# Optimization experiments

Measured on AMD Instinct MI355X. Metric: run time of the kernel, lower is better.

## Reference

```python
import jax, jax.numpy as jnp
import numpy as np

N, NFEAT, NHID, NCLASS, NHEADS = 8192, 512, 64, 16, 4
ALPHA = 0.2          # leaky_relu slope for attention scores
OUT_SLOPE = 0.01     # flax default slope for per-head output leaky_relu
NEG = -9000000000000000.0


def glorot(key, shape):
    fan_in, fan_out = shape[0], shape[1]
    lim = jnp.sqrt(6.0 / (fan_in + fan_out))
    return jax.random.uniform(key, shape, jnp.float32, -lim, lim)


def setup_inputs() -> dict:
    key = jax.random.key(0)
    ks = jax.random.split(key, 6)
    x = jax.random.normal(ks[0], (N, NFEAT), jnp.float32)
    adj = jax.random.randint(ks[1], (N, N), 0, 2, jnp.int32)
    Wh = glorot(ks[2], (NHEADS * NFEAT, NHID)).reshape(NHEADS, NFEAT, NHID)
    ah = glorot(ks[3], (NHEADS * 2 * NHID, 1)).reshape(NHEADS, 2 * NHID, 1)
    Wo = glorot(ks[4], (NHID * NHEADS, NCLASS))
    ao = glorot(ks[5], (2 * NCLASS, 1))
    return {"x": x, "adj": adj, "Wh": Wh, "ah": ah, "Wo": Wo, "ao": ao}


def _gat_layer(x, adj_mask, W, a, score_slope):
    # h: (N, F)
    h = x @ W
    F = h.shape[1]
    # a_input[i,j] = concat(h_i, h_j); a_input @ a == f1[i] + f2[j]
    f1 = h @ a[:F, 0]   # (N,)
    f2 = h @ a[F:, 0]   # (N,)
    e = jax.nn.leaky_relu(f1[:, None] + f2[None, :], negative_slope=score_slope)
    att = jax.nn.softmax(jnp.where(adj_mask, e, NEG), axis=1)  # (N, N)
    return att @ h  # (N, F)


def reference(x, adj, Wh, ah, Wo, ao):
    adj_mask = adj > 0
    heads = []
    for k in range(NHEADS):  # small fixed structural loop
        hp = _gat_layer(x, adj_mask, Wh[k], ah[k], ALPHA)
        heads.append(jax.nn.leaky_relu(hp, negative_slope=OUT_SLOPE))
    xcat = jnp.concatenate(heads, axis=1)  # (N, NHEADS*NHID)
    # output head: concat=False -> return h_prime directly
    return _gat_layer(xcat, adj_mask, Wo, ao, ALPHA)  # (N, NCLASS)
```

## Files before the change

kernel.cpp:

```cpp
#include <hip/hip_runtime.h>
#include <stdint.h>

#define N      8192
#define FEAT   512
#define HID    64
#define NH     4
#define C1     256
#define PCH    80
#define TC     320
#define NCLS   16
#define C2     32
#define IPB    8

typedef __attribute__((ext_vector_type(8))) short bf16x8;
typedef __attribute__((ext_vector_type(4))) float f32x4;

__device__ __forceinline__ float b2f(uint16_t u){
  uint32_t x = ((uint32_t)u) << 16;
  return __builtin_bit_cast(float, x);
}
__device__ __forceinline__ uint16_t f2b(float f){
  uint32_t x = __builtin_bit_cast(uint32_t, f);
  uint32_t r = (x + 0x7fffu + ((x >> 16) & 1u)) >> 16;
  return (uint16_t)r;
}
__device__ __forceinline__ float lrelu(float v, float a){ return fmaxf(v, a * v); }

__global__ void k0_wht(const float* __restrict__ Wh, float* __restrict__ WhT){
  int idx = blockIdx.x * 256 + threadIdx.x;
  int k = idx >> 15;
  int r = idx & 32767;
  int cc = r >> 9, f = r & 511;
  WhT[idx] = Wh[k * 32768 + f * 64 + cc];
}

__global__ __launch_bounds__(256) void k1_h(const float* __restrict__ x,
    const float* __restrict__ WhT, const float* __restrict__ ah,
    uint16_t* __restrict__ H, float* __restrict__ f1, float* __restrict__ f2)
{
  __shared__ float4 xs[IPB][128];
  int t = threadIdx.x;
  int i0 = blockIdx.x * IPB;
  for (int r = t; r < IPB * 128; r += 256){
    int ii = r >> 7, o = r & 127;
    xs[ii][o] = *((const float4*)(x + (size_t)(i0 + ii) * FEAT) + o);
  }
  __syncthreads();
  int k = t >> 6, cc = t & 63;
  const float4* wrow = (const float4*)(WhT + k * 32768 + cc * 512);
  float acc[IPB] = {};
  for (int f4 = 0; f4 < 128; ++f4){
    float4 wv = wrow[f4];
    #pragma unroll
    for (int ii = 0; ii < IPB; ++ii){
      float4 xv = xs[ii][f4];
      acc[ii] += xv.x * wv.x + xv.y * wv.y + xv.z * wv.z + xv.w * wv.w;
    }
  }
  float a1 = ah[k * 128 + cc], a2 = ah[k * 128 + 64 + cc];
  #pragma unroll
  for (int ii = 0; ii < IPB; ++ii){
    int i = i0 + ii;
    H[(size_t)i * C1 + t] = f2b(acc[ii]);
    float c1v = acc[ii] * a1, c2v = acc[ii] * a2;
    #pragma unroll
    for (int off = 32; off; off >>= 1){
      c1v += __shfl_down(c1v, off);
      c2v += __shfl_down(c2v, off);
    }
    if (cc == 0){ f1[k * N + i] = c1v; f2[k * N + i] = c2v; }
  }
}

__global__ void k2a_htT(const uint16_t* __restrict__ H, uint16_t* __restrict__ HT){
  __shared__ uint16_t tile[64][65];
  int bid = blockIdx.x;
  int k = bid & 3, it = bid >> 2;
  int i0 = it * 64;
  int t = threadIdx.x;
  #pragma unroll
  for (int r = 0; r < 4; ++r){
    int ii = r * 16 + (t >> 4);
    int pp = (t & 15) * 4;
    uint2 v = *(const uint2*)(H + (size_t)(i0 + ii) * C1 + k * 64 + pp);
    const uint16_t* s = (const uint16_t*)&v;
    tile[pp + 0][ii] = s[0]; tile[pp + 1][ii] = s[1];
    tile[pp + 2][ii] = s[2]; tile[pp + 3][ii] = s[3];
  }
  __syncthreads();
  #pragma unroll
  for (int r = 0; r < 4; ++r){
    int pp = r * 16 + (t >> 4);
    int ii = (t & 15) * 4;
    uint2 v;
    uint16_t* s = (uint16_t*)&v;
    s[0] = tile[pp][ii + 0]; s[1] = tile[pp][ii + 1];
    s[2] = tile[pp][ii + 2]; s[3] = tile[pp][ii + 3];
    *(uint2*)(HT + (size_t)k * (PCH * N) + (size_t)pp * N + i0 + ii) = v;
  }
}

__global__ void k2b_fill(uint16_t* __restrict__ HT){
  int fidx = blockIdx.x * 256 + threadIdx.x;
  int k = fidx >> 14;
  int rem = fidx & 16383;
  int p = 64 + (rem >> 10);
  int i0 = (rem & 1023) << 3;
  uint32_t w = (p == 64) ? 0x3F803F80u : 0u;
  uint4 v = {w, w, w, w};
  *((uint4*)(HT + (size_t)k * (PCH * N) + (size_t)p * N + i0)) = v;
}

__global__ __launch_bounds__(256, 2) void k3_attA(const int* __restrict__ adj,
    const uint16_t* __restrict__ HT, const float* __restrict__ f1,
    const float* __restrict__ f2, float* __restrict__ accA)
{
  __shared__ uint16_t Pl[NH][64][48];
  __shared__ uint16_t Hl[TC][48];
  __shared__ float f1s[NH][64];

  const int t = threadIdx.x;
  const int ibl = blockIdx.x >> 2;
  const int js = blockIdx.x & 3;
  const int gi0 = ibl * 64;

  { int k = t >> 6, ii = t & 63; f1s[k][ii] = f1[k * N + gi0 + ii]; }

  const int tj   = t & 31;
  const int half = t >> 5;
  const int lane = t & 63;
  const int wid  = t >> 6;
  const int m    = lane & 15;
  const int q    = lane >> 4;

  f32x4 acc[4][5] = {};
  const int* arow0 = adj + (size_t)(gi0 + half) * N + tj;

  for (int jc = 0; jc < 64; ++jc){
    const int gj = js * 2048 + jc * 32;
    float f2v0 = f2[0 * N + gj + tj];
    float f2v1 = f2[1 * N + gj + tj];
    float f2v2 = f2[2 * N + gj + tj];
    float f2v3 = f2[3 * N + gj + tj];
    int av[8];
    #pragma unroll
    for (int r = 0; r < 8; ++r) av[r] = arow0[(size_t)(8 * r) * N + gj];

    __syncthreads();
    #pragma unroll
    for (int r = 0; r < 5; ++r){
      int idx = t + 256 * r;
      int p = idx >> 2, o4 = idx & 3;
      *(uint4*)&Hl[p][o4 * 8] = *(const uint4*)(HT + (size_t)p * N + gj + o4 * 8);
    }
    #pragma unroll
    for (int r = 0; r < 8; ++r){
      int i = half + 8 * r;
      int a = av[r];
      float s0 = f1s[0][i] + f2v0;
      float s1 = f1s[1][i] + f2v1;
      float s2 = f1s[2][i] + f2v2;
      float s3 = f1s[3][i] + f2v3;
      float w0 = (a > 0) ? __expf(lrelu(s0, 0.2f)) : 0.f;
      float w1 = (a > 0) ? __expf(lrelu(s1, 0.2f)) : 0.f;
      float w2 = (a > 0) ? __expf(lrelu(s2, 0.2f)) : 0.f;
      float w3 = (a > 0) ? __expf(lrelu(s3, 0.2f)) : 0.f;
      Pl[0][i][tj] = f2b(w0);
      Pl[1][i][tj] = f2b(w1);
      Pl[2][i][tj] = f2b(w2);
      Pl[3][i][tj] = f2b(w3);
    }
    __syncthreads();

    bf16x8 af[4];
    #pragma unroll
    for (int it = 0; it < 4; ++it)
      af[it] = *(const bf16x8*)&Pl[wid][it * 16 + m][q * 8];
    #pragma unroll
    for (int ct = 0; ct < 5; ++ct){
      bf16x8 bfr = *(const bf16x8*)&Hl[wid * PCH + ct * 16 + m][q * 8];
      #pragma unroll
      for (int it = 0; it < 4; ++it)
        acc[it][ct] = __builtin_amdgcn_mfma_f32_16x16x32_bf16(af[it], bfr, acc[it][ct], 0, 0, 0);
    }
  }

  #pragma unroll
  for (int it = 0; it < 4; ++it)
    #pragma unroll
    for (int ct = 0; ct < 5; ++ct)
      #pragma unroll
      for (int reg = 0; reg < 4; ++reg){
        int gi = gi0 + it * 16 + q * 4 + reg;
        int c  = wid * PCH + ct * 16 + m;
        accA[((size_t)js * N + gi) * TC + c] = acc[it][ct][reg];
      }
}

__global__ void k4_redA(const float* __restrict__ accA, uint16_t* __restrict__ xcat){
  int i = blockIdx.x;
  int t = threadIdx.x;
  int k = t >> 6, cc = t & 63;
  size_t base = (size_t)i * TC + k * PCH;
  float v = 0.f, Z = 0.f;
  #pragma unroll
  for (int js = 0; js < 4; ++js){
    const float* p = accA + (size_t)js * N * TC + base;
    v += p[cc];
    Z += p[64];
  }
  float r = v / Z;
  xcat[(size_t)i * C1 + t] = f2b(lrelu(r, 0.01f));
}

__global__ __launch_bounds__(256) void k5_h2(const uint16_t* __restrict__ xcat,
    const float* __restrict__ Wo, const float* __restrict__ ao,
    uint16_t* __restrict__ h2T, float* __restrict__ f1o, float* __restrict__ f2o)
{
  __shared__ uint16_t xs[16][256];
  int t = threadIdx.x;
  int i0 = blockIdx.x * 16;
  #pragma unroll
  for (int r = 0; r < 2; ++r){
    int idx = t + 256 * r;
    int ii = idx >> 5, o4 = idx & 31;
    *(uint4*)&xs[ii][o4 * 8] = *(const uint4*)(xcat + (size_t)(i0 + ii) * C1 + o4 * 8);
  }
  __syncthreads();
  int ii = t >> 4, c = t & 15;
  float acc = 0.f;
  for (int f = 0; f < 256; ++f)
    acc += b2f(xs[ii][f]) * Wo[f * 16 + c];
  int i = i0 + ii;
  h2T[(size_t)c * N + i] = f2b(acc);
  float u1 = acc * ao[c];
  float u2 = acc * ao[16 + c];
  #pragma unroll
  for (int off = 8; off; off >>= 1){
    u1 += __shfl_down(u1, off, 16);
    u2 += __shfl_down(u2, off, 16);
  }
  if (c == 0){ f1o[i] = u1; f2o[i] = u2; }
  if (t < 16) h2T[(size_t)16 * N + i0 + t] = 0x3F80;
  if (t < 240){
    int p = 17 + t / 16, io = t % 16;
    h2T[(size_t)p * N + i0 + io] = 0;
  }
}

__global__ __launch_bounds__(256) void k6_attB(const int* __restrict__ adj,
    const uint16_t* __restrict__ h2T, const float* __restrict__ f1o,
    const float* __restrict__ f2o, float* __restrict__ accB)
{
  __shared__ uint16_t Pl[64][48];
  __shared__ uint16_t Hl[32][48];
  __shared__ float f1s[64];

  const int t = threadIdx.x;
  const int ibl = blockIdx.x >> 3;
  const int js = blockIdx.x & 7;
  const int gi0 = ibl * 64;
  if (t < 64) f1s[t] = f1o[gi0 + t];

  const int tj = t & 31;
  const int half = t >> 5;
  const int lane = t & 63;
  const int wid = t >> 6;
  const int m = lane & 15;
  const int q = lane >> 4;

  f32x4 acc0 = {0.f, 0.f, 0.f, 0.f}, acc1 = {0.f, 0.f, 0.f, 0.f};
  const int* arow0 = adj + (size_t)(gi0 + half) * N + tj;

  for (int jc = 0; jc < 32; ++jc){
    const int gj = js * 1024 + jc * 32;
    float f2v = f2o[gj + tj];
    int av[8];
    #pragma unroll
    for (int r = 0; r < 8; ++r) av[r] = arow0[(size_t)(8 * r) * N + gj];

    __syncthreads();
    if (t < 128){
      int p = t >> 2, o4 = t & 3;
      *(uint4*)&Hl[p][o4 * 8] = *(const uint4*)(h2T + (size_t)p * N + gj + o4 * 8);
    }
    #pragma unroll
    for (int r = 0; r < 8; ++r){
      int i = half + 8 * r;
      float s = f1s[i] + f2v;
      float w = (av[r] > 0) ? __expf(lrelu(s, 0.2f)) : 0.f;
      Pl[i][tj] = f2b(w);
    }
    __syncthreads();

    bf16x8 af = *(const bf16x8*)&Pl[wid * 16 + m][q * 8];
    bf16x8 b0 = *(const bf16x8*)&Hl[m][q * 8];
    bf16x8 b1 = *(const bf16x8*)&Hl[16 + m][q * 8];
    acc0 = __builtin_amdgcn_mfma_f32_16x16x32_bf16(af, b0, acc0, 0, 0, 0);
    acc1 = __builtin_amdgcn_mfma_f32_16x16x32_bf16(af, b1, acc1, 0, 0, 0);
  }

  #pragma unroll
  for (int reg = 0; reg < 4; ++reg){
    int gi = gi0 + wid * 16 + q * 4 + reg;
    accB[((size_t)js * N + gi) * C2 + m] = acc0[reg];
    accB[((size_t)js * N + gi) * C2 + 16 + m] = acc1[reg];
  }
}

__global__ void k7_redB(const float* __restrict__ accB, float* __restrict__ out){
  int idx = blockIdx.x * 256 + threadIdx.x;
  int i = idx >> 4, c = idx & 15;
  float v = 0.f, Z = 0.f;
  #pragma unroll
  for (int js = 0; js < 8; ++js){
    const float* p = accB + ((size_t)js * N + i) * C2;
    v += p[c];
    Z += p[16];
  }
  out[idx] = v / Z;
}

extern "C" void kernel_launch(void* const* d_in, const int* in_sizes, int n_in,
                              void* d_out, int out_size, void* d_ws, size_t ws_size,
                              hipStream_t stream)
{
  const float* x   = (const float*)d_in[0];
  const int*   adj = (const int*)d_in[1];
  const float* Wh  = (const float*)d_in[2];
  const float* ah  = (const float*)d_in[3];
  const float* Wo  = (const float*)d_in[4];
  const float* ao  = (const float*)d_in[5];
  float* out = (float*)d_out;

  char* ws = (char*)d_ws;
  float*    WhT  = (float*)   (ws);
  uint16_t* H    = (uint16_t*)(ws + 524288);
  uint16_t* HT   = (uint16_t*)(ws + 4718592);
  float*    f1   = (float*)   (ws + 9961472);
  float*    f2   = (float*)   (ws + 10092544);
  float*    accA = (float*)   (ws + 10223616);
  uint16_t* xcat = (uint16_t*)(ws + 52166656);
  uint16_t* h2T  = (uint16_t*)(ws + 56360960);
  float*    f1o  = (float*)   (ws + 56885248);
  float*    f2o  = (float*)   (ws + 56918016);
  float*    accB = (float*)   (ws + 56950784);

  hipLaunchKernelGGL(k0_wht,   dim3(512),  dim3(256), 0, stream, Wh, WhT);
  hipLaunchKernelGGL(k1_h,     dim3(1024), dim3(256), 0, stream, x, WhT, ah, H, f1, f2);
  hipLaunchKernelGGL(k2a_htT,  dim3(512),  dim3(256), 0, stream, H, HT);
  hipLaunchKernelGGL(k2b_fill, dim3(256),  dim3(256), 0, stream, HT);
  hipLaunchKernelGGL(k3_attA,  dim3(512),  dim3(256), 0, stream, adj, HT, f1, f2, accA);
  hipLaunchKernelGGL(k4_redA,  dim3(8192), dim3(256), 0, stream, accA, xcat);
  hipLaunchKernelGGL(k5_h2,    dim3(512),  dim3(256), 0, stream, xcat, Wo, ao, h2T, f1o, f2o);
  hipLaunchKernelGGL(k6_attB,  dim3(1024), dim3(256), 0, stream, adj, h2T, f1o, f2o, accB);
  hipLaunchKernelGGL(k7_redB,  dim3(512),  dim3(256), 0, stream, accB, out);
}
```

Measured before the change: 631.1 us.

## Bit-pack adjacency, factor exp scores, prefetch tiles in attention kernels

Adds a pre-pass that compresses the int32 adjacency matrix into a transposed bitmask. Both attention kernels then read one bit per edge instead of a full int, which removes most of their adjacency traffic. Attention weights are now built as products of precomputed exp(f1)·exp(f2) and exp(0.2f1)·exp(0.2f2), picking the branch by comparing against 1, so no per-edge exp is needed. The first attention kernel is split across head pairs to double the grid, and next-tile loads are software-prefetched into registers. The price is an extra adjacency conversion pass, possible overflow or precision loss in the exp products, and truncating bf16 rounding.

```diff
diff --git a/kernel.cpp b/kernel.cpp
--- a/kernel.cpp
+++ b/kernel.cpp
@@ -8,7 +8,6 @@
 #define C1     256
 #define PCH    80
 #define TC     320
-#define NCLS   16
 #define C2     32
 #define IPB    8
 
@@ -24,7 +23,29 @@
   uint32_t r = (x + 0x7fffu + ((x >> 16) & 1u)) >> 16;
   return (uint16_t)r;
 }
-__device__ __forceinline__ float lrelu(float v, float a){ return fmaxf(v, a * v); }
+__device__ __forceinline__ uint32_t pack_bf2(float a, float b){
+  uint32_t ua = (__builtin_bit_cast(uint32_t, a) + 0x8000u) >> 16;
+  uint32_t ub = (__builtin_bit_cast(uint32_t, b) + 0x8000u) & 0xFFFF0000u;
+  return ua | ub;
+}
+
+__global__ __launch_bounds__(256) void kA_bits(const int* __restrict__ adj, uint32_t* __restrict__ adjbT){
+  int bid = blockIdx.x;
+  int iband = bid & 127, jwq = bid >> 7;
+  int t = threadIdx.x;
+  int i  = iband * 64 + (t & 63);
+  int jw = jwq * 4 + (t >> 6);
+  const int4* ap = (const int4*)(adj + (size_t)i * N + jw * 32);
+  uint32_t w = 0;
+  #pragma unroll
+  for (int e = 0; e < 8; ++e){
+    int4 v = ap[e];
+    uint32_t nib = (uint32_t)(v.x & 1) | ((uint32_t)(v.y & 1) << 1)
+                 | ((uint32_t)(v.z & 1) << 2) | ((uint32_t)(v.w & 1) << 3);
+    w |= nib << (4 * e);
+  }
+  adjbT[(size_t)jw * N + i] = w;
+}
 
 __global__ void k0_wht(const float* __restrict__ Wh, float* __restrict__ WhT){
   int idx = blockIdx.x * 256 + threadIdx.x;
@@ -72,6 +93,14 @@
   }
 }
 
+__global__ void kE_exp(const float* __restrict__ f1, const float* __restrict__ f2,
+                       float2* __restrict__ e1p, float2* __restrict__ e2p){
+  int idx = blockIdx.x * 256 + threadIdx.x;
+  float v1 = f1[idx], v2 = f2[idx];
+  e1p[idx] = make_float2(__expf(v1), __expf(0.2f * v1));
+  e2p[idx] = make_float2(__expf(v2), __expf(0.2f * v2));
+}
+
 __global__ void k2a_htT(const uint16_t* __restrict__ H, uint16_t* __restrict__ HT){
   __shared__ uint16_t tile[64][65];
   int bid = blockIdx.x;
@@ -111,88 +140,137 @@
   *((uint4*)(HT + (size_t)k * (PCH * N) + (size_t)p * N + i0)) = v;
 }
 
-__global__ __launch_bounds__(256, 2) void k3_attA(const int* __restrict__ adj,
-    const uint16_t* __restrict__ HT, const float* __restrict__ f1,
-    const float* __restrict__ f2, float* __restrict__ accA)
+__global__ __launch_bounds__(256) void k3_attA(const uint32_t* __restrict__ adjbT,
+    const uint16_t* __restrict__ HT, const float* __restrict__ e1p,
+    const float* __restrict__ e2p, float* __restrict__ accA)
 {
-  __shared__ uint16_t Pl[NH][64][48];
-  __shared__ uint16_t Hl[TC][48];
-  __shared__ float f1s[NH][64];
-
-  const int t = threadIdx.x;
-  const int ibl = blockIdx.x >> 2;
-  const int js = blockIdx.x & 3;
+  __shared__ uint16_t Pl[2][64][40];
+  __shared__ uint16_t Hl[160][40];
+
+  const int t   = threadIdx.x;
+  const int bid = blockIdx.x;
+  const int js  = bid & 3;
+  const int hp  = (bid >> 2) & 1;
+  const int ibl = bid >> 3;
   const int gi0 = ibl * 64;
 
-  { int k = t >> 6, ii = t & 63; f1s[k][ii] = f1[k * N + gi0 + ii]; }
-
-  const int tj   = t & 31;
-  const int half = t >> 5;
+  const int jp = t & 15;
+  const int rg = t >> 4;
   const int lane = t & 63;
   const int wid  = t >> 6;
+  const int h_w  = wid >> 1;
+  const int ihalf= wid & 1;
   const int m    = lane & 15;
   const int q    = lane >> 4;
 
-  f32x4 acc[4][5] = {};
-  const int* arow0 = adj + (size_t)(gi0 + half) * N + tj;
-
-  for (int jc = 0; jc < 64; ++jc){
-    const int gj = js * 2048 + jc * 32;
-    float f2v0 = f2[0 * N + gj + tj];
-    float f2v1 = f2[1 * N + gj + tj];
-    float f2v2 = f2[2 * N + gj + tj];
-    float f2v3 = f2[3 * N + gj + tj];
-    int av[8];
-    #pragma unroll
-    for (int r = 0; r < 8; ++r) av[r] = arow0[(size_t)(8 * r) * N + gj];
-
-    __syncthreads();
-    #pragma unroll
-    for (int r = 0; r < 5; ++r){
+  float2 e1v[2][4];
+  #pragma unroll
+  for (int h = 0; h < 2; ++h)
+    #pragma unroll
+    for (int rr = 0; rr < 4; ++rr)
+      e1v[h][rr] = ((const float2*)e1p)[(size_t)(hp * 2 + h) * N + gi0 + rg + 16 * rr];
+
+  f32x4 acc[2][5] = {};
+
+  uint4  vht[3];
+  uint32_t mw[4];
+  float4 e2q[2];
+
+  const int NJ = 64;
+  {
+    const int gj = js * 2048;
+    const int jw = gj >> 5;
+    #pragma unroll
+    for (int r = 0; r < 3; ++r){
       int idx = t + 256 * r;
       int p = idx >> 2, o4 = idx & 3;
-      *(uint4*)&Hl[p][o4 * 8] = *(const uint4*)(HT + (size_t)p * N + gj + o4 * 8);
-    }
-    #pragma unroll
-    for (int r = 0; r < 8; ++r){
-      int i = half + 8 * r;
-      int a = av[r];
-      float s0 = f1s[0][i] + f2v0;
-      float s1 = f1s[1][i] + f2v1;
-      float s2 = f1s[2][i] + f2v2;
-      float s3 = f1s[3][i] + f2v3;
-      float w0 = (a > 0) ? __expf(lrelu(s0, 0.2f)) : 0.f;
-      float w1 = (a > 0) ? __expf(lrelu(s1, 0.2f)) : 0.f;
-      float w2 = (a > 0) ? __expf(lrelu(s2, 0.2f)) : 0.f;
-      float w3 = (a > 0) ? __expf(lrelu(s3, 0.2f)) : 0.f;
-      Pl[0][i][tj] = f2b(w0);
-      Pl[1][i][tj] = f2b(w1);
-      Pl[2][i][tj] = f2b(w2);
-      Pl[3][i][tj] = f2b(w3);
-    }
+      if (r < 2 || t < 128)
+        vht[r] = *(const uint4*)(HT + (size_t)(hp * 160 + p) * N + gj + o4 * 8);
+    }
+    #pragma unroll
+    for (int rr = 0; rr < 4; ++rr)
+      mw[rr] = adjbT[(size_t)jw * N + gi0 + rg + 16 * rr];
+    #pragma unroll
+    for (int h = 0; h < 2; ++h)
+      e2q[h] = *(((const float4*)e2p) + (((size_t)(hp * 2 + h) * N + gj) >> 1) + jp);
+  }
+
+  for (int jc = 0; jc < NJ; ++jc){
+    uint32_t pk[2][4];
+    #pragma unroll
+    for (int h = 0; h < 2; ++h){
+      float4 q4 = e2q[h];
+      #pragma unroll
+      for (int rr = 0; rr < 4; ++rr){
+        float2 e1 = e1v[h][rr];
+        float pa = e1.x * q4.x, psa = e1.y * q4.y;
+        float pb = e1.x * q4.z, psb = e1.y * q4.w;
+        float wa = pa > 1.0f ? pa : psa;
+        float wb = pb > 1.0f ? pb : psb;
+        uint32_t sh = mw[rr] >> (2 * jp);
+        wa = (sh & 1u) ? wa : 0.0f;
+        wb = (sh & 2u) ? wb : 0.0f;
+        pk[h][rr] = pack_bf2(wa, wb);
+      }
+    }
+
     __syncthreads();
-
-    bf16x8 af[4];
-    #pragma unroll
-    for (int it = 0; it < 4; ++it)
-      af[it] = *(const bf16x8*)&Pl[wid][it * 16 + m][q * 8];
+    #pragma unroll
+    for (int r = 0; r < 3; ++r){
+      int idx = t + 256 * r;
+      int p = idx >> 2, o4 = idx & 3;
+      if (r < 2 || t < 128)
+        *(uint4*)&Hl[p][o4 * 8] = vht[r];
+    }
+    {
+      uint32_t* Plw = (uint32_t*)Pl;
+      #pragma unroll
+      for (int h = 0; h < 2; ++h)
+        #pragma unroll
+        for (int rr = 0; rr < 4; ++rr)
+          Plw[(h * 64 + rg + 16 * rr) * 20 + jp] = pk[h][rr];
+    }
+    {
+      int jn = (jc + 1 < NJ) ? jc + 1 : jc;
+      const int gj = js * 2048 + jn * 32;
+      const int jw = gj >> 5;
+      #pragma unroll
+      for (int r = 0; r < 3; ++r){
+        int idx = t + 256 * r;
+        int p = idx >> 2, o4 = idx & 3;
+        if (r < 2 || t < 128)
+          vht[r] = *(const uint4*)(HT + (size_t)(hp * 160 + p) * N + gj + o4 * 8);
+      }
+      #pragma unroll
+      for (int rr = 0; rr < 4; ++rr)
+        mw[rr] = adjbT[(size_t)jw * N + gi0 + rg + 16 * rr];
+      #pragma unroll
+      for (int h = 0; h < 2; ++h)
+        e2q[h] = *(((const float4*)e2p) + (((size_t)(hp * 2 + h) * N + gj) >> 1) + jp);
+    }
+    __syncthreads();
+
+    bf16x8 af[2];
+    #pragma unroll
+    for (int it = 0; it < 2; ++it)
+      af[it] = *(const bf16x8*)&Pl[h_w][ihalf * 32 + it * 16 + m][q * 8];
     #pragma unroll
     for (int ct = 0; ct < 5; ++ct){
-      bf16x8 bfr = *(const bf16x8*)&Hl[wid * PCH + ct * 16 + m][q * 8];
-      #pragma unroll
-      for (int it = 0; it < 4; ++it)
+      bf16x8 bfr = *(const bf16x8*)&Hl[h_w * 80 + ct * 16 + m][q * 8];
+      #pragma unroll
+      for (int it = 0; it < 2; ++it)
         acc[it][ct] = __builtin_amdgcn_mfma_f32_16x16x32_bf16(af[it], bfr, acc[it][ct], 0, 0, 0);
     }
   }
 
   #pragma unroll
-  for (int it = 0; it < 4; ++it)
+  for (int it = 0; it < 2; ++it)
     #pragma unroll
     for (int ct = 0; ct < 5; ++ct)
       #pragma unroll
       for (int reg = 0; reg < 4; ++reg){
-        int gi = gi0 + it * 16 + q * 4 + reg;
-        int c  = wid * PCH + ct * 16 + m;
+        int gi = gi0 + ihalf * 32 + it * 16 + q * 4 + reg;
+        int c  = (hp * 2 + h_w) * PCH + ct * 16 + m;
         accA[((size_t)js * N + gi) * TC + c] = acc[it][ct][reg];
       }
 }
@@ -210,12 +288,12 @@
     Z += p[64];
   }
   float r = v / Z;
-  xcat[(size_t)i * C1 + t] = f2b(lrelu(r, 0.01f));
+  xcat[(size_t)i * C1 + t] = f2b(fmaxf(r, 0.01f * r));
 }
 
 __global__ __launch_bounds__(256) void k5_h2(const uint16_t* __restrict__ xcat,
     const float* __restrict__ Wo, const float* __restrict__ ao,
-    uint16_t* __restrict__ h2T, float* __restrict__ f1o, float* __restrict__ f2o)
+    uint16_t* __restrict__ h2T, float2* __restrict__ e1op, float2* __restrict__ e2op)
 {
   __shared__ uint16_t xs[16][256];
   int t = threadIdx.x;
@@ -240,7 +318,10 @@
     u1 += __shfl_down(u1, off, 16);
     u2 += __shfl_down(u2, off, 16);
   }
-  if (c == 0){ f1o[i] = u1; f2o[i] = u2; }
+  if (c == 0){
+    e1op[i] = make_float2(__expf(u1), __expf(0.2f * u1));
+    e2op[i] = make_float2(__expf(u2), __expf(0.2f * u2));
+  }
   if (t < 16) h2T[(size_t)16 * N + i0 + t] = 0x3F80;
   if (t < 240){
     int p = 17 + t / 16, io = t % 16;
@@ -248,64 +329,112 @@
   }
 }
 
-__global__ __launch_bounds__(256) void k6_attB(const int* __restrict__ adj,
-    const uint16_t* __restrict__ h2T, const float* __restrict__ f1o,
-    const float* __restrict__ f2o, float* __restrict__ accB)
+__global__ __launch_bounds__(256) void k6_attB(const uint32_t* __restrict__ adjbT,
+    const uint16_t* __restrict__ h2T, const float* __restrict__ e1op,
+    const float* __restrict__ e2op, float* __restrict__ accB)
 {
-  __shared__ uint16_t Pl[64][48];
-  __shared__ uint16_t Hl[32][48];
-  __shared__ float f1s[64];
-
-  const int t = threadIdx.x;
-  const int ibl = blockIdx.x >> 3;
-  const int js = blockIdx.x & 7;
+  __shared__ uint16_t Pl[64][40];
+  __shared__ uint16_t Hl[32][40];
+
+  const int t   = threadIdx.x;
+  const int bid = blockIdx.x;
+  const int js  = bid & 7;
+  const int ibl = bid >> 3;
   const int gi0 = ibl * 64;
-  if (t < 64) f1s[t] = f1o[gi0 + t];
-
-  const int tj = t & 31;
-  const int half = t >> 5;
+
+  const int jp = t & 15;
+  const int rg = t >> 4;
   const int lane = t & 63;
-  const int wid = t >> 6;
-  const int m = lane & 15;
-  const int q = lane >> 4;
-
-  f32x4 acc0 = {0.f, 0.f, 0.f, 0.f}, acc1 = {0.f, 0.f, 0.f, 0.f};
-  const int* arow0 = adj + (size_t)(gi0 + half) * N + tj;
-
-  for (int jc = 0; jc < 32; ++jc){
-    const int gj = js * 1024 + jc * 32;
-    float f2v = f2o[gj + tj];
-    int av[8];
-    #pragma unroll
-    for (int r = 0; r < 8; ++r) av[r] = arow0[(size_t)(8 * r) * N + gj];
+  const int wid  = t >> 6;
+  const int ihalf= wid & 1;
+  const int chalf= wid >> 1;
+  const int m    = lane & 15;
+  const int q    = lane >> 4;
+
+  float2 e1v[4];
+  #pragma unroll
+  for (int rr = 0; rr < 4; ++rr)
+    e1v[rr] = ((const float2*)e1op)[gi0 + rg + 16 * rr];
+
+  f32x4 acc[2] = {};
+
+  uint4 vht;
+  uint32_t mw[4];
+  float4 e2q;
+
+  const int NJ = 32;
+  {
+    const int gj = js * 1024;
+    const int jw = gj >> 5;
+    if (t < 128){
+      int p = t >> 2, o4 = t & 3;
+      vht = *(const uint4*)(h2T + (size_t)p * N + gj + o4 * 8);
+    }
+    #pragma unroll
+    for (int rr = 0; rr < 4; ++rr)
+      mw[rr] = adjbT[(size_t)jw * N + gi0 + rg + 16 * rr];
+    e2q = *(((const float4*)e2op) + (gj >> 1) + jp);
+  }
+
+  for (int jc = 0; jc < NJ; ++jc){
+    uint32_t pk[4];
+    {
+      float4 q4 = e2q;
+      #pragma unroll
+      for (int rr = 0; rr < 4; ++rr){
+        float2 e1 = e1v[rr];
+        float pa = e1.x * q4.x, psa = e1.y * q4.y;
+        float pb = e1.x * q4.z, psb = e1.y * q4.w;
+        float wa = pa > 1.0f ? pa : psa;
+        float wb = pb > 1.0f ? pb : psb;
+        uint32_t sh = mw[rr] >> (2 * jp);
+        wa = (sh & 1u) ? wa : 0.0f;
+        wb = (sh & 2u) ? wb : 0.0f;
+        pk[rr] = pack_bf2(wa, wb);
+      }
+    }
 
     __syncthreads();
     if (t < 128){
       int p = t >> 2, o4 = t & 3;
-      *(uint4*)&Hl[p][o4 * 8] = *(const uint4*)(h2T + (size_t)p * N + gj + o4 * 8);
-    }
-    #pragma unroll
-    for (int r = 0; r < 8; ++r){
-      int i = half + 8 * r;
-      float s = f1s[i] + f2v;
-      float w = (av[r] > 0) ? __expf(lrelu(s, 0.2f)) : 0.f;
-      Pl[i][tj] = f2b(w);
+      *(uint4*)&Hl[p][o4 * 8] = vht;
+    }
+    {
+      uint32_t* Plw = (uint32_t*)Pl;
+      #pragma unroll
+      for (int rr = 0; rr < 4; ++rr)
+        Plw[(rg + 16 * rr) * 20 + jp] = pk[rr];
+    }
+    {
+      int jn = (jc + 1 < NJ) ? jc + 1 : jc;
+      const int gj = js * 1024 + jn * 32;
+      const int jw = gj >> 5;
+      if (t < 128){
+        int p = t >> 2, o4 = t & 3;
+        vht = *(const uint4*)(h2T + (size_t)p * N + gj + o4 * 8);
+      }
+      #pragma unroll
+      for (int rr = 0; rr < 4; ++rr)
+        mw[rr] = adjbT[(size_t)jw * N + gi0 + rg + 16 * rr];
+      e2q = *(((const float4*)e2op) + (gj >> 1) + jp);
     }
     __syncthreads();
 
-    bf16x8 af = *(const bf16x8*)&Pl[wid * 16 + m][q * 8];
-    bf16x8 b0 = *(const bf16x8*)&Hl[m][q * 8];
-    bf16x8 b1 = *(const bf16x8*)&Hl[16 + m][q * 8];
-    acc0 = __builtin_amdgcn_mfma_f32_16x16x32_bf16(af, b0, acc0, 0, 0, 0);
-    acc1 = __builtin_amdgcn_mfma_f32_16x16x32_bf16(af, b1, acc1, 0, 0, 0);
-  }
-
-  #pragma unroll
-  for (int reg = 0; reg < 4; ++reg){
-    int gi = gi0 + wid * 16 + q * 4 + reg;
-    accB[((size_t)js * N + gi) * C2 + m] = acc0[reg];
-    accB[((size_t)js * N + gi) * C2 + 16 + m] = acc1[reg];
-  }
+    bf16x8 bfr = *(const bf16x8*)&Hl[chalf * 16 + m][q * 8];
+    #pragma unroll
+    for (int it = 0; it < 2; ++it){
+      bf16x8 af = *(const bf16x8*)&Pl[ihalf * 32 + it * 16 + m][q * 8];
+      acc[it] = __builtin_amdgcn_mfma_f32_16x16x32_bf16(af, bfr, acc[it], 0, 0, 0);
+    }
+  }
+
+  #pragma unroll
+  for (int it = 0; it < 2; ++it)
+    #pragma unroll
+    for (int reg = 0; reg < 4; ++reg){
+      int gi = gi0 + ihalf * 32 + it * 16 + q * 4 + reg;
+      accB[((size_t)js * N + gi) * C2 + chalf * 16 + m] = acc[it][reg];
+    }
 }
 
 __global__ void k7_redB(const float* __restrict__ accB, float* __restrict__ out){
@@ -334,25 +463,30 @@
   float* out = (float*)d_out;
 
   char* ws = (char*)d_ws;
-  float*    WhT  = (float*)   (ws);
-  uint16_t* H    = (uint16_t*)(ws + 524288);
-  uint16_t* HT   = (uint16_t*)(ws + 4718592);
-  float*    f1   = (float*)   (ws + 9961472);
-  float*    f2   = (float*)   (ws + 10092544);
-  float*    accA = (float*)   (ws + 10223616);
-  uint16_t* xcat = (uint16_t*)(ws + 52166656);
-  uint16_t* h2T  = (uint16_t*)(ws + 56360960);
-  float*    f1o  = (float*)   (ws + 56885248);
-  float*    f2o  = (float*)   (ws + 56918016);
-  float*    accB = (float*)   (ws + 56950784);
-
+  float*    WhT   = (float*)   (ws);
+  uint16_t* H     = (uint16_t*)(ws + 524288);
+  uint16_t* HT    = (uint16_t*)(ws + 4718592);
+  float*    f1    = (float*)   (ws + 9961472);
+  float*    f2    = (float*)   (ws + 10092544);
+  float*    accA  = (float*)   (ws + 10223616);
+  uint16_t* xcat  = (uint16_t*)(ws + 52166656);
+  uint16_t* h2T   = (uint16_t*)(ws + 56360960);
+  float2*   e1op  = (float2*)  (ws + 56885248);
+  float2*   e2op  = (float2*)  (ws + 56950784);
+  float*    accB  = (float*)   (ws + 57016320);
+  float2*   e1p   = (float2*)  (ws + 65404928);
+  float2*   e2p   = (float2*)  (ws + 65667072);
+  uint32_t* adjbT = (uint32_t*)(ws + 65929216);
+
+  hipLaunchKernelGGL(kA_bits,  dim3(8192), dim3(256), 0, stream, adj, adjbT);
   hipLaunchKernelGGL(k0_wht,   dim3(512),  dim3(256), 0, stream, Wh, WhT);
   hipLaunchKernelGGL(k1_h,     dim3(1024), dim3(256), 0, stream, x, WhT, ah, H, f1, f2);
+  hipLaunchKernelGGL(kE_exp,   dim3(128),  dim3(256), 0, stream, f1, f2, e1p, e2p);
   hipLaunchKernelGGL(k2a_htT,  dim3(512),  dim3(256), 0, stream, H, HT);
   hipLaunchKernelGGL(k2b_fill, dim3(256),  dim3(256), 0, stream, HT);
-  hipLaunchKernelGGL(k3_attA,  dim3(512),  dim3(256), 0, stream, adj, HT, f1, f2, accA);
+  hipLaunchKernelGGL(k3_attA,  dim3(1024), dim3(256), 0, stream, adjbT, HT, (const float*)e1p, (const float*)e2p, accA);
   hipLaunchKernelGGL(k4_redA,  dim3(8192), dim3(256), 0, stream, accA, xcat);
-  hipLaunchKernelGGL(k5_h2,    dim3(512),  dim3(256), 0, stream, xcat, Wo, ao, h2T, f1o, f2o);
-  hipLaunchKernelGGL(k6_attB,  dim3(1024), dim3(256), 0, stream, adj, h2T, f1o, f2o, accB);
+  hipLaunchKernelGGL(k5_h2,    dim3(512),  dim3(256), 0, stream, xcat, Wo, ao, h2T, e1op, e2op);
+  hipLaunchKernelGGL(k6_attB,  dim3(1024), dim3(256), 0, stream, adjbT, h2T, (const float*)e1op, (const float*)e2op, accB);
   hipLaunchKernelGGL(k7_redB,  dim3(512),  dim3(256), 0, stream, accB, out);
 }
```

New measurement: 740.8 us. 17.4% more time.

## Bit-pack adjacency and factor exp of attention scores into per-node products

Applied to the files above, without the earlier changes.

Adds a pre-pass that packs the int32 adjacency matrix into a transposed bitmask, so both attention kernels read 32x less adjacency data. It rewrites exp(leaky_relu(f1+f2)) as max(e^f1·e^f2, e^{0.2f1}·e^{0.2f2}) using precomputed per-node exponentials, which removes the per-edge exp. The attention kernels now build the MFMA A fragments in registers and load the H fragments straight from global memory, dropping the LDS staging and barriers. The grid is restructured to one head per block. Possible costs are overflow when exponentials are computed separately, and bf16 rounding that now skips the tie-to-even step.

```diff
diff --git a/kernel.cpp b/kernel.cpp
--- a/kernel.cpp
+++ b/kernel.cpp
@@ -8,12 +8,12 @@
 #define C1     256
 #define PCH    80
 #define TC     320
-#define NCLS   16
 #define C2     32
 #define IPB    8
 
 typedef __attribute__((ext_vector_type(8))) short bf16x8;
 typedef __attribute__((ext_vector_type(4))) float f32x4;
+typedef __attribute__((ext_vector_type(4))) uint32_t u32x4;
 
 __device__ __forceinline__ float b2f(uint16_t u){
   uint32_t x = ((uint32_t)u) << 16;
@@ -24,7 +24,29 @@
   uint32_t r = (x + 0x7fffu + ((x >> 16) & 1u)) >> 16;
   return (uint16_t)r;
 }
-__device__ __forceinline__ float lrelu(float v, float a){ return fmaxf(v, a * v); }
+__device__ __forceinline__ uint32_t pack_bf2(float a, float b){
+  uint32_t ua = (__builtin_bit_cast(uint32_t, a) + 0x8000u) >> 16;
+  uint32_t ub = (__builtin_bit_cast(uint32_t, b) + 0x8000u) & 0xFFFF0000u;
+  return ua | ub;
+}
+
+__global__ __launch_bounds__(256) void kA_bits(const int* __restrict__ adj, uint32_t* __restrict__ adjbT){
+  int bid = blockIdx.x;
+  int iband = bid & 127, jwq = bid >> 7;
+  int t = threadIdx.x;
+  int i  = iband * 64 + (t & 63);
+  int jw = jwq * 4 + (t >> 6);
+  const int4* ap = (const int4*)(adj + (size_t)i * N + jw * 32);
+  uint32_t w = 0;
+  #pragma unroll
+  for (int e = 0; e < 8; ++e){
+    int4 v = ap[e];
+    uint32_t nib = (uint32_t)(v.x & 1) | ((uint32_t)(v.y & 1) << 1)
+                 | ((uint32_t)(v.z & 1) << 2) | ((uint32_t)(v.w & 1) << 3);
+    w |= nib << (4 * e);
+  }
+  adjbT[(size_t)jw * N + i] = w;
+}
 
 __global__ void k0_wht(const float* __restrict__ Wh, float* __restrict__ WhT){
   int idx = blockIdx.x * 256 + threadIdx.x;
@@ -70,6 +92,14 @@
     }
     if (cc == 0){ f1[k * N + i] = c1v; f2[k * N + i] = c2v; }
   }
+}
+
+__global__ void kE_exp(const float* __restrict__ f1, const float* __restrict__ f2,
+                       float2* __restrict__ e1p, float2* __restrict__ e2p){
+  int idx = blockIdx.x * 256 + threadIdx.x;
+  float v1 = f1[idx], v2 = f2[idx];
+  e1p[idx] = make_float2(__expf(v1), __expf(0.2f * v1));
+  e2p[idx] = make_float2(__expf(v2), __expf(0.2f * v2));
 }
 
 __global__ void k2a_htT(const uint16_t* __restrict__ H, uint16_t* __restrict__ HT){
@@ -111,88 +141,79 @@
   *((uint4*)(HT + (size_t)k * (PCH * N) + (size_t)p * N + i0)) = v;
 }
 
-__global__ __launch_bounds__(256, 2) void k3_attA(const int* __restrict__ adj,
-    const uint16_t* __restrict__ HT, const float* __restrict__ f1,
-    const float* __restrict__ f2, float* __restrict__ accA)
-{
-  __shared__ uint16_t Pl[NH][64][48];
-  __shared__ uint16_t Hl[TC][48];
-  __shared__ float f1s[NH][64];
-
-  const int t = threadIdx.x;
-  const int ibl = blockIdx.x >> 2;
-  const int js = blockIdx.x & 3;
-  const int gi0 = ibl * 64;
-
-  { int k = t >> 6, ii = t & 63; f1s[k][ii] = f1[k * N + gi0 + ii]; }
-
-  const int tj   = t & 31;
-  const int half = t >> 5;
+__global__ __launch_bounds__(256) void k3_attA(const uint32_t* __restrict__ adjbT,
+    const uint16_t* __restrict__ HT, const float2* __restrict__ e1p,
+    const float2* __restrict__ e2p, float* __restrict__ accA)
+{
+  const int t    = threadIdx.x;
+  const int bid  = blockIdx.x;
+  const int js   = bid & 3;
+  const int head = (bid >> 2) & 3;
+  const int ig   = bid >> 4;
+  const int w    = t >> 6;
   const int lane = t & 63;
-  const int wid  = t >> 6;
   const int m    = lane & 15;
   const int q    = lane >> 4;
-
-  f32x4 acc[4][5] = {};
-  const int* arow0 = adj + (size_t)(gi0 + half) * N + tj;
+  const int gi0  = ig * 128 + w * 32;
+
+  float2 e1v0 = e1p[(size_t)head * N + gi0 + m];
+  float2 e1v1 = e1p[(size_t)head * N + gi0 + 16 + m];
+
+  const uint16_t* Hbase = HT + (size_t)head * (PCH * N) + (size_t)m * N + q * 8;
+  const float2*   E2b   = e2p + (size_t)head * N;
+  const uint32_t* Mb0   = adjbT + gi0 + m;
+  const uint32_t* Mb1   = adjbT + gi0 + 16 + m;
+
+  f32x4 acc[2][5] = {};
 
   for (int jc = 0; jc < 64; ++jc){
     const int gj = js * 2048 + jc * 32;
-    float f2v0 = f2[0 * N + gj + tj];
-    float f2v1 = f2[1 * N + gj + tj];
-    float f2v2 = f2[2 * N + gj + tj];
-    float f2v3 = f2[3 * N + gj + tj];
-    int av[8];
-    #pragma unroll
-    for (int r = 0; r < 8; ++r) av[r] = arow0[(size_t)(8 * r) * N + gj];
-
-    __syncthreads();
-    #pragma unroll
-    for (int r = 0; r < 5; ++r){
-      int idx = t + 256 * r;
-      int p = idx >> 2, o4 = idx & 3;
-      *(uint4*)&Hl[p][o4 * 8] = *(const uint4*)(HT + (size_t)p * N + gj + o4 * 8);
-    }
-    #pragma unroll
-    for (int r = 0; r < 8; ++r){
-      int i = half + 8 * r;
-      int a = av[r];
-      float s0 = f1s[0][i] + f2v0;
-      float s1 = f1s[1][i] + f2v1;
-      float s2 = f1s[2][i] + f2v2;
-      float s3 = f1s[3][i] + f2v3;
-      float w0 = (a > 0) ? __expf(lrelu(s0, 0.2f)) : 0.f;
-      float w1 = (a > 0) ? __expf(lrelu(s1, 0.2f)) : 0.f;
-      float w2 = (a > 0) ? __expf(lrelu(s2, 0.2f)) : 0.f;
-      float w3 = (a > 0) ? __expf(lrelu(s3, 0.2f)) : 0.f;
-      Pl[0][i][tj] = f2b(w0);
-      Pl[1][i][tj] = f2b(w1);
-      Pl[2][i][tj] = f2b(w2);
-      Pl[3][i][tj] = f2b(w3);
-    }
-    __syncthreads();
-
-    bf16x8 af[4];
-    #pragma unroll
-    for (int it = 0; it < 4; ++it)
-      af[it] = *(const bf16x8*)&Pl[wid][it * 16 + m][q * 8];
+    const int jw = gj >> 5;
+    const float4* E2 = (const float4*)(E2b + gj);
+    float4 ev[4];
+    #pragma unroll
+    for (int r = 0; r < 4; ++r) ev[r] = E2[q * 4 + r];
+    uint32_t mw0 = Mb0[(size_t)jw * N];
+    uint32_t mw1 = Mb1[(size_t)jw * N];
+    bf16x8 bq[5];
+    #pragma unroll
+    for (int ct = 0; ct < 5; ++ct)
+      bq[ct] = *(const bf16x8*)(Hbase + (size_t)(ct * 16) * N + gj);
+
+    uint32_t sh0 = mw0 >> (q * 8);
+    uint32_t sh1 = mw1 >> (q * 8);
+    u32x4 pk0, pk1;
+    #pragma unroll
+    for (int p = 0; p < 4; ++p){
+      float4 v = ev[p];
+      float wa0 = fmaxf(e1v0.x * v.x, e1v0.y * v.y);
+      float wb0 = fmaxf(e1v0.x * v.z, e1v0.y * v.w);
+      wa0 = ((sh0 >> (2 * p)) & 1u) ? wa0 : 0.f;
+      wb0 = ((sh0 >> (2 * p)) & 2u) ? wb0 : 0.f;
+      pk0[p] = pack_bf2(wa0, wb0);
+      float wa1 = fmaxf(e1v1.x * v.x, e1v1.y * v.y);
+      float wb1 = fmaxf(e1v1.x * v.z, e1v1.y * v.w);
+      wa1 = ((sh1 >> (2 * p)) & 1u) ? wa1 : 0.f;
+      wb1 = ((sh1 >> (2 * p)) & 2u) ? wb1 : 0.f;
+      pk1[p] = pack_bf2(wa1, wb1);
+    }
+    bf16x8 af0 = __builtin_bit_cast(bf16x8, pk0);
+    bf16x8 af1 = __builtin_bit_cast(bf16x8, pk1);
     #pragma unroll
     for (int ct = 0; ct < 5; ++ct){
-      bf16x8 bfr = *(const bf16x8*)&Hl[wid * PCH + ct * 16 + m][q * 8];
-      #pragma unroll
-      for (int it = 0; it < 4; ++it)
-        acc[it][ct] = __builtin_amdgcn_mfma_f32_16x16x32_bf16(af[it], bfr, acc[it][ct], 0, 0, 0);
-    }
-  }
-
-  #pragma unroll
-  for (int it = 0; it < 4; ++it)
+      acc[0][ct] = __builtin_amdgcn_mfma_f32_16x16x32_bf16(af0, bq[ct], acc[0][ct], 0, 0, 0);
+      acc[1][ct] = __builtin_amdgcn_mfma_f32_16x16x32_bf16(af1, bq[ct], acc[1][ct], 0, 0, 0);
+    }
+  }
+
+  #pragma unroll
+  for (int it = 0; it < 2; ++it)
     #pragma unroll
     for (int ct = 0; ct < 5; ++ct)
       #pragma unroll
       for (int reg = 0; reg < 4; ++reg){
         int gi = gi0 + it * 16 + q * 4 + reg;
-        int c  = wid * PCH + ct * 16 + m;
+        int c  = head * PCH + ct * 16 + m;
         accA[((size_t)js * N + gi) * TC + c] = acc[it][ct][reg];
       }
 }
@@ -210,12 +231,12 @@
     Z += p[64];
   }
   float r = v / Z;
-  xcat[(size_t)i * C1 + t] = f2b(lrelu(r, 0.01f));
+  xcat[(size_t)i * C1 + t] = f2b(fmaxf(r, 0.01f * r));
 }
 
 __global__ __launch_bounds__(256) void k5_h2(const uint16_t* __restrict__ xcat,
     const float* __restrict__ Wo, const float* __restrict__ ao,
-    uint16_t* __restrict__ h2T, float* __restrict__ f1o, float* __restrict__ f2o)
+    uint16_t* __restrict__ h2T, float2* __restrict__ e1op, float2* __restrict__ e2op)
 {
   __shared__ uint16_t xs[16][256];
   int t = threadIdx.x;
@@ -240,7 +261,10 @@
     u1 += __shfl_down(u1, off, 16);
     u2 += __shfl_down(u2, off, 16);
   }
-  if (c == 0){ f1o[i] = u1; f2o[i] = u2; }
+  if (c == 0){
+    e1op[i] = make_float2(__expf(u1), __expf(0.2f * u1));
+    e2op[i] = make_float2(__expf(u2), __expf(0.2f * u2));
+  }
   if (t < 16) h2T[(size_t)16 * N + i0 + t] = 0x3F80;
   if (t < 240){
     int p = 17 + t / 16, io = t % 16;
@@ -248,64 +272,61 @@
   }
 }
 
-__global__ __launch_bounds__(256) void k6_attB(const int* __restrict__ adj,
-    const uint16_t* __restrict__ h2T, const float* __restrict__ f1o,
-    const float* __restrict__ f2o, float* __restrict__ accB)
-{
-  __shared__ uint16_t Pl[64][48];
-  __shared__ uint16_t Hl[32][48];
-  __shared__ float f1s[64];
-
-  const int t = threadIdx.x;
-  const int ibl = blockIdx.x >> 3;
-  const int js = blockIdx.x & 7;
-  const int gi0 = ibl * 64;
-  if (t < 64) f1s[t] = f1o[gi0 + t];
-
-  const int tj = t & 31;
-  const int half = t >> 5;
+__global__ __launch_bounds__(128) void k6_attB(const uint32_t* __restrict__ adjbT,
+    const uint16_t* __restrict__ h2T, const float2* __restrict__ e1op,
+    const float2* __restrict__ e2op, float* __restrict__ accB)
+{
+  const int t    = threadIdx.x;
+  const int bid  = blockIdx.x;
+  const int js   = bid & 7;
+  const int ig   = bid >> 3;
+  const int w    = t >> 6;
   const int lane = t & 63;
-  const int wid = t >> 6;
-  const int m = lane & 15;
-  const int q = lane >> 4;
-
-  f32x4 acc0 = {0.f, 0.f, 0.f, 0.f}, acc1 = {0.f, 0.f, 0.f, 0.f};
-  const int* arow0 = adj + (size_t)(gi0 + half) * N + tj;
-
+  const int m    = lane & 15;
+  const int q    = lane >> 4;
+  const int gi0  = (ig * 2 + w) * 16;
+
+  float2 e1v = e1op[gi0 + m];
+  const uint16_t* Hbase = h2T + (size_t)m * N + q * 8;
+  const uint32_t* Mb    = adjbT + gi0 + m;
+
+  f32x4 acc[2] = {};
+
+  #pragma unroll 2
   for (int jc = 0; jc < 32; ++jc){
     const int gj = js * 1024 + jc * 32;
-    float f2v = f2o[gj + tj];
-    int av[8];
-    #pragma unroll
-    for (int r = 0; r < 8; ++r) av[r] = arow0[(size_t)(8 * r) * N + gj];
-
-    __syncthreads();
-    if (t < 128){
-      int p = t >> 2, o4 = t & 3;
-      *(uint4*)&Hl[p][o4 * 8] = *(const uint4*)(h2T + (size_t)p * N + gj + o4 * 8);
-    }
-    #pragma unroll
-    for (int r = 0; r < 8; ++r){
-      int i = half + 8 * r;
-      float s = f1s[i] + f2v;
-      float w = (av[r] > 0) ? __expf(lrelu(s, 0.2f)) : 0.f;
-      Pl[i][tj] = f2b(w);
-    }
-    __syncthreads();
-
-    bf16x8 af = *(const bf16x8*)&Pl[wid * 16 + m][q * 8];
-    bf16x8 b0 = *(const bf16x8*)&Hl[m][q * 8];
-    bf16x8 b1 = *(const bf16x8*)&Hl[16 + m][q * 8];
-    acc0 = __builtin_amdgcn_mfma_f32_16x16x32_bf16(af, b0, acc0, 0, 0, 0);
-    acc1 = __builtin_amdgcn_mfma_f32_16x16x32_bf16(af, b1, acc1, 0, 0, 0);
-  }
-
-  #pragma unroll
-  for (int reg = 0; reg < 4; ++reg){
-    int gi = gi0 + wid * 16 + q * 4 + reg;
-    accB[((size_t)js * N + gi) * C2 + m] = acc0[reg];
-    accB[((size_t)js * N + gi) * C2 + 16 + m] = acc1[reg];
-  }
+    const int jw = gj >> 5;
+    const float4* E2 = (const float4*)(e2op + gj);
+    float4 ev[4];
+    #pragma unroll
+    for (int r = 0; r < 4; ++r) ev[r] = E2[q * 4 + r];
+    uint32_t mw = Mb[(size_t)jw * N];
+    bf16x8 bq0 = *(const bf16x8*)(Hbase + gj);
+    bf16x8 bq1 = *(const bf16x8*)(Hbase + (size_t)16 * N + gj);
+
+    uint32_t sh = mw >> (q * 8);
+    u32x4 pk;
+    #pragma unroll
+    for (int p = 0; p < 4; ++p){
+      float4 v = ev[p];
+      float wa = fmaxf(e1v.x * v.x, e1v.y * v.y);
+      float wb = fmaxf(e1v.x * v.z, e1v.y * v.w);
+      wa = ((sh >> (2 * p)) & 1u) ? wa : 0.f;
+      wb = ((sh >> (2 * p)) & 2u) ? wb : 0.f;
+      pk[p] = pack_bf2(wa, wb);
+    }
+    bf16x8 af = __builtin_bit_cast(bf16x8, pk);
+    acc[0] = __builtin_amdgcn_mfma_f32_16x16x32_bf16(af, bq0, acc[0], 0, 0, 0);
+    acc[1] = __builtin_amdgcn_mfma_f32_16x16x32_bf16(af, bq1, acc[1], 0, 0, 0);
+  }
+
+  #pragma unroll
+  for (int ct = 0; ct < 2; ++ct)
+    #pragma unroll
+    for (int reg = 0; reg < 4; ++reg){
+      int gi = gi0 + q * 4 + reg;
+      accB[((size_t)js * N + gi) * C2 + ct * 16 + m] = acc[ct][reg];
+    }
 }
 
 __global__ void k7_redB(const float* __restrict__ accB, float* __restrict__ out){
@@ -334,25 +355,30 @@
   float* out = (float*)d_out;
 
   char* ws = (char*)d_ws;
-  float*    WhT  = (float*)   (ws);
-  uint16_t* H    = (uint16_t*)(ws + 524288);
-  uint16_t* HT   = (uint16_t*)(ws + 4718592);
-  float*    f1   = (float*)   (ws + 9961472);
-  float*    f2   = (float*)   (ws + 10092544);
-  float*    accA = (float*)   (ws + 10223616);
-  uint16_t* xcat = (uint16_t*)(ws + 52166656);
-  uint16_t* h2T  = (uint16_t*)(ws + 56360960);
-  float*    f1o  = (float*)   (ws + 56885248);
-  float*    f2o  = (float*)   (ws + 56918016);
-  float*    accB = (float*)   (ws + 56950784);
-
+  float*    WhT   = (float*)   (ws);
+  uint16_t* H     = (uint16_t*)(ws + 524288);
+  uint16_t* HT    = (uint16_t*)(ws + 4718592);
+  float*    f1    = (float*)   (ws + 9961472);
+  float*    f2    = (float*)   (ws + 10092544);
+  float*    accA  = (float*)   (ws + 10223616);
+  uint16_t* xcat  = (uint16_t*)(ws + 52166656);
+  uint16_t* h2T   = (uint16_t*)(ws + 56360960);
+  float2*   e1op  = (float2*)  (ws + 56885248);
+  float2*   e2op  = (float2*)  (ws + 56950784);
+  float*    accB  = (float*)   (ws + 57016320);
+  float2*   e1p   = (float2*)  (ws + 65404928);
+  float2*   e2p   = (float2*)  (ws + 65667072);
+  uint32_t* adjbT = (uint32_t*)(ws + 65929216);
+
+  hipLaunchKernelGGL(kA_bits,  dim3(8192), dim3(256), 0, stream, adj, adjbT);
   hipLaunchKernelGGL(k0_wht,   dim3(512),  dim3(256), 0, stream, Wh, WhT);
   hipLaunchKernelGGL(k1_h,     dim3(1024), dim3(256), 0, stream, x, WhT, ah, H, f1, f2);
+  hipLaunchKernelGGL(kE_exp,   dim3(128),  dim3(256), 0, stream, f1, f2, e1p, e2p);
   hipLaunchKernelGGL(k2a_htT,  dim3(512),  dim3(256), 0, stream, H, HT);
   hipLaunchKernelGGL(k2b_fill, dim3(256),  dim3(256), 0, stream, HT);
-  hipLaunchKernelGGL(k3_attA,  dim3(512),  dim3(256), 0, stream, adj, HT, f1, f2, accA);
+  hipLaunchKernelGGL(k3_attA,  dim3(1024), dim3(256), 0, stream, adjbT, HT, e1p, e2p, accA);
   hipLaunchKernelGGL(k4_redA,  dim3(8192), dim3(256), 0, stream, accA, xcat);
-  hipLaunchKernelGGL(k5_h2,    dim3(512),  dim3(256), 0, stream, xcat, Wo, ao, h2T, f1o, f2o);
-  hipLaunchKernelGGL(k6_attB,  dim3(1024), dim3(256), 0, stream, adj, h2T, f1o, f2o, accB);
+  hipLaunchKernelGGL(k5_h2,    dim3(512),  dim3(256), 0, stream, xcat, Wo, ao, h2T, e1op, e2op);
+  hipLaunchKernelGGL(k6_attB,  dim3(2048), dim3(128), 0, stream, adjbT, h2T, e1op, e2op, accB);
   hipLaunchKernelGGL(k7_redB,  dim3(512),  dim3(256), 0, stream, accB, out);
 }
```

New measurement: 774.4 us. 22.7% more time.
